# Performance work log

Hardware: AMD Instinct MI355X
Metric: run time of the kernel (lower is better)

Reference implementation:

```python
import jax, jax.numpy as jnp
import numpy as np

D_MODEL = 1024

def setup_inputs() -> dict:
    key = jax.random.key(0)
    k1, k2, kU, kb, kw, kfb = jax.random.split(key, 6)
    B, S, d = 8, 2048, D_MODEL
    x1 = jax.random.normal(k1, (B, S, d), dtype=jnp.float32)
    x2 = jax.random.normal(k2, (B, S, d), dtype=jnp.float32)
    U = jax.random.normal(kU, (d, d), dtype=jnp.float32) * (1.0 / np.sqrt(d))
    bias = jax.random.normal(kb, (d,), dtype=jnp.float32) * 0.02
    fc_w = jax.random.normal(kw, (d // 2, d), dtype=jnp.float32) * (1.0 / np.sqrt(d))
    fc_b = jnp.zeros((d // 2,), dtype=jnp.float32)
    return {"x1": x1, "x2": x2, "U": U, "bias": bias, "fc_w": fc_w, "fc_b": fc_b}

def reference(x1, x2, U, bias, fc_w, fc_b):
    # attn scores: (x2 @ U) @ x1^T  -> [B, S2, S1]
    attn = jnp.einsum("bsd,de,bte->bst", x2, U, x1)
    # additive bias per key position: x1 @ bias -> [B, 1, S1]
    attn = attn + jnp.einsum("btd,d->bt", x1, bias)[:, None, :]
    attn = jax.nn.softmax(attn, axis=-1)
    # dropout is identity in eval mode
    out = jnp.einsum("bst,btd->bsd", attn, x1)
    out = jnp.einsum("bsd,ed->bse", out, fc_w) + fc_b
    return jax.nn.relu(out)
```

## Files before the change

### kernel.cpp

```cpp
#include <hip/hip_runtime.h>
#include <hip/hip_fp16.h>
#include <cstddef>
#include <cstdint>

typedef _Float16 f16;
typedef _Float16 f16x8 __attribute__((ext_vector_type(8)));
typedef _Float16 f16x4 __attribute__((ext_vector_type(4)));
typedef float    f32x4 __attribute__((ext_vector_type(4)));

#define BK 64

__device__ __forceinline__ void gload16(const void* g, void* lds) {
  __builtin_amdgcn_global_load_lds(
      (const __attribute__((address_space(1))) unsigned int*)g,
      (__attribute__((address_space(3))) unsigned int*)lds, 16, 0, 0);
}

template<int R>
__device__ __forceinline__ void stage_f16(f16 (*buf)[BK], const f16* __restrict__ src,
                                          int ld, int w, int lane) {
#pragma unroll
  for (int i = 0; i < R / 32; i++) {
    const int grp  = w * (R / 32) + i;
    const int r    = grp * 8 + (lane >> 3);
    const int slot = (lane & 7) ^ (r & 7);
    gload16(src + (size_t)r * ld + slot * 8, &buf[grp * 8][0]);
  }
}

template<int R>
struct RegStage {
  static constexpr int NV = (R == 128) ? 8 : 4;
  float4 v[NV];
  __device__ __forceinline__ void load(const float* __restrict__ src, int ld, int tid) {
    const int r = (R == 128) ? (tid >> 1) : (tid >> 2);
    const int h = (R == 128) ? (tid & 1) * 32 : (tid & 3) * 16;
    const float* p = src + (size_t)r * ld + h;
#pragma unroll
    for (int j = 0; j < NV; j++) v[j] = ((const float4*)p)[j];
  }
  __device__ __forceinline__ void write(f16 (*buf)[BK], int tid) {
    const int r = (R == 128) ? (tid >> 1) : (tid >> 2);
    const int h = (R == 128) ? (tid & 1) * 32 : (tid & 3) * 16;
#pragma unroll
    for (int g = 0; g < NV / 2; g++) {
      const float4 a = v[g * 2], b = v[g * 2 + 1];
      f16x8 o;
      o[0] = (f16)a.x; o[1] = (f16)a.y; o[2] = (f16)a.z; o[3] = (f16)a.w;
      o[4] = (f16)b.x; o[5] = (f16)b.y; o[6] = (f16)b.z; o[7] = (f16)b.w;
      const int slot = (h / 8 + g) ^ (r & 7);
      *(f16x8*)&buf[r][slot * 8] = o;
    }
  }
};

template<int BMt, int BNt, typename TA, typename TB, bool BIAS, bool RELU, typename TC>
__global__ __launch_bounds__(256, 2)
void gemm_tn(const TA* __restrict__ A, int lda,
             const TB* __restrict__ B, int ldb,
             TC* __restrict__ C, int ldc,
             const float* __restrict__ bias, int K)
{
  constexpr int MF = BMt / 32;
  constexpr int NF = BNt / 32;
  __shared__ f16 As[2][BMt][BK];
  __shared__ f16 Bs[2][BNt][BK];
  const int tid  = threadIdx.x;
  const int lane = tid & 63;
  const int w    = tid >> 6;
  const int wr   = w >> 1, wc = w & 1;

  const int gx = gridDim.x, nxy = gx * gridDim.y;
  int lin = blockIdx.y * gx + blockIdx.x;
  lin = (lin & 7) * (nxy >> 3) + (lin >> 3);
  const int m0 = (lin % gx) * BMt;
  const int n0 = (lin / gx) * BNt;

  f32x4 acc[MF][NF] = {};
  RegStage<BMt> ra;
  RegStage<BNt> rb;

  auto stage_issue = [&](int buf, int k0) {
    if constexpr (sizeof(TA) == 2)
      stage_f16<BMt>(As[buf], (const f16*)A + (size_t)m0 * lda + k0, lda, w, lane);
    else
      ra.load((const float*)A + (size_t)m0 * lda + k0, lda, tid);
    if constexpr (sizeof(TB) == 2)
      stage_f16<BNt>(Bs[buf], (const f16*)B + (size_t)n0 * ldb + k0, ldb, w, lane);
    else
      rb.load((const float*)B + (size_t)n0 * ldb + k0, ldb, tid);
  };
  auto stage_write = [&](int buf) {
    if constexpr (sizeof(TA) == 4) ra.write(As[buf], tid);
    if constexpr (sizeof(TB) == 4) rb.write(Bs[buf], tid);
  };
  auto compute = [&](int buf) {
    const int fr = lane & 15, q = lane >> 4;
#pragma unroll
    for (int kk = 0; kk < 2; kk++) {
      f16x8 af[MF], bf[NF];
#pragma unroll
      for (int i = 0; i < MF; i++) {
        const int r = wr * (BMt / 2) + i * 16 + fr;
        const int slot = (kk * 4 + q) ^ (r & 7);
        af[i] = *(const f16x8*)&As[buf][r][slot * 8];
      }
#pragma unroll
      for (int j = 0; j < NF; j++) {
        const int r = wc * (BNt / 2) + j * 16 + fr;
        const int slot = (kk * 4 + q) ^ (r & 7);
        bf[j] = *(const f16x8*)&Bs[buf][r][slot * 8];
      }
#pragma unroll
      for (int i = 0; i < MF; i++)
#pragma unroll
        for (int j = 0; j < NF; j++)
          acc[i][j] = __builtin_amdgcn_mfma_f32_16x16x32_f16(af[i], bf[j], acc[i][j], 0, 0, 0);
    }
  };

  stage_issue(0, 0);
  stage_write(0);
  __syncthreads();

  const int KT = K / BK;
  for (int kt = 0; kt < KT; kt++) {
    const int cur = kt & 1, nxt = cur ^ 1;
    if (kt + 1 < KT) stage_issue(nxt, (kt + 1) * BK);
    compute(cur);
    if (kt + 1 < KT) stage_write(nxt);
    __syncthreads();
  }

  const int fr = lane & 15;
  const int rg = (lane >> 4) << 2;
#pragma unroll
  for (int i = 0; i < MF; i++) {
#pragma unroll
    for (int j = 0; j < NF; j++) {
      const int col = n0 + wc * (BNt / 2) + j * 16 + fr;
      float bv = 0.f;
      if constexpr (BIAS) bv = bias[col];
#pragma unroll
      for (int r = 0; r < 4; r++) {
        const int row = m0 + wr * (BMt / 2) + i * 16 + rg + r;
        float v = acc[i][j][r] + bv;
        if constexpr (RELU) v = fmaxf(v, 0.f);
        C[(size_t)row * ldc + col] = (TC)v;
      }
    }
  }
}

__global__ __launch_bounds__(256)
void copy_f32_f16(const float* __restrict__ in, f16* __restrict__ o)
{
  const size_t i = ((size_t)blockIdx.x * 256 + threadIdx.x) * 8;
  const float4 a = ((const float4*)(in + i))[0];
  const float4 b = ((const float4*)(in + i))[1];
  f16x8 v;
  v[0] = (f16)a.x; v[1] = (f16)a.y; v[2] = (f16)a.z; v[3] = (f16)a.w;
  v[4] = (f16)b.x; v[5] = (f16)b.y; v[6] = (f16)b.z; v[7] = (f16)b.w;
  *(f16x8*)(o + i) = v;
}

__global__ __launch_bounds__(256)
void bias_dot(const float* __restrict__ x1, const float* __restrict__ bias,
              float* __restrict__ bT)
{
  const int row  = blockIdx.x * 4 + (threadIdx.x >> 6);
  const int lane = threadIdx.x & 63;
  const float4* r = (const float4*)(x1 + (size_t)row * 1024);
  const float4* bb = (const float4*)bias;
  float acc = 0.f;
#pragma unroll
  for (int j = 0; j < 4; j++) {
    const float4 a = r[lane + j * 64];
    const float4 b = bb[lane + j * 64];
    acc += a.x * b.x + a.y * b.y + a.z * b.z + a.w * b.w;
  }
#pragma unroll
  for (int off = 32; off > 0; off >>= 1) acc += __shfl_xor(acc, off);
  if (lane == 0) bT[row] = acc;
}

__global__ __launch_bounds__(256)
void softmax_rows(float* __restrict__ S)
{
  float* row = S + (size_t)blockIdx.x * 2048;
  const int t = threadIdx.x;
  const float4 v0 = ((const float4*)row)[t];
  const float4 v1 = ((const float4*)row)[t + 256];

  float m = fmaxf(fmaxf(fmaxf(v0.x, v0.y), fmaxf(v0.z, v0.w)),
                  fmaxf(fmaxf(v1.x, v1.y), fmaxf(v1.z, v1.w)));
#pragma unroll
  for (int off = 32; off > 0; off >>= 1) m = fmaxf(m, __shfl_xor(m, off));
  __shared__ float red[8];
  if ((t & 63) == 0) red[t >> 6] = m;
  __syncthreads();
  m = fmaxf(fmaxf(red[0], red[1]), fmaxf(red[2], red[3]));

  float e0 = __expf(v0.x - m), e1 = __expf(v0.y - m), e2 = __expf(v0.z - m), e3 = __expf(v0.w - m);
  float e4 = __expf(v1.x - m), e5 = __expf(v1.y - m), e6 = __expf(v1.z - m), e7 = __expf(v1.w - m);
  float s = ((e0 + e1) + (e2 + e3)) + ((e4 + e5) + (e6 + e7));
#pragma unroll
  for (int off = 32; off > 0; off >>= 1) s += __shfl_xor(s, off);
  if ((t & 63) == 0) red[4 + (t >> 6)] = s;
  __syncthreads();
  const float inv = 1.f / (red[4] + red[5] + red[6] + red[7]);

  f16x4 o0, o1;
  o0[0] = (f16)(e0 * inv); o0[1] = (f16)(e1 * inv); o0[2] = (f16)(e2 * inv); o0[3] = (f16)(e3 * inv);
  o1[0] = (f16)(e4 * inv); o1[1] = (f16)(e5 * inv); o1[2] = (f16)(e6 * inv); o1[3] = (f16)(e7 * inv);
  f16x4* orow = (f16x4*)row;
  orow[t]       = o0;
  orow[t + 256] = o1;
}

extern "C" void kernel_launch(void* const* d_in, const int* in_sizes, int n_in,
                              void* d_out, int out_size, void* d_ws, size_t ws_size,
                              hipStream_t stream)
{
  const float* x1   = (const float*)d_in[0];
  const float* x2   = (const float*)d_in[1];
  const float* U    = (const float*)d_in[2];
  const float* bias = (const float*)d_in[3];
  const float* fcw  = (const float*)d_in[4];
  const float* fcb  = (const float*)d_in[5];
  float* out = (float*)d_out;

  const int S = 2048, D = 1024, E = 512, B = 8;
  const size_t MB = 1ull << 20;
  const size_t KB64 = 64 * 1024;

  const bool FULL = ws_size >= (4 * MB + KB64 + 16 * MB);

  char* w = (char*)d_ws;
  f16*   W2  = (f16*)(w);
  f16*   W1Tf = (f16*)(w + 4 * MB);
  float* bT  = FULL ? (float*)(w + 4 * MB) : (float*)(w + 6 * MB);
  float* Sb  = FULL ? (float*)(w + 4 * MB + KB64) : (float*)(w + 6 * MB + KB64);
  f16*   Uh  = (f16*)(w + 14 * MB + KB64);
  f16*   Fh  = (f16*)(w + 16 * MB + KB64);

  const int SC = FULL ? 2048 : 1024;

  f16* X2h = (f16*)d_out;

  copy_f32_f16<<<dim3(B * S * D / 2048), 256, 0, stream>>>(x2, X2h);
  bias_dot<<<dim3(B * S / 4), 256, 0, stream>>>(x1, bias, bT);
  if (!FULL) {
    copy_f32_f16<<<dim3(D * D / 2048), 256, 0, stream>>>(U, Uh);
    copy_f32_f16<<<dim3(E * D / 2048), 256, 0, stream>>>(fcw, Fh);
  }

  for (int b = 0; b < B; b++) {
    const float* x1b = x1 + (size_t)b * S * D;
    const f16*   X2b = X2h + (size_t)b * S * D;

    if (FULL) {
      gemm_tn<64, 128, float, float, false, false, f16><<<dim3(S / 64, D / 128), 256, 0, stream>>>(
          x1b, D, U, D, W2, D, nullptr, D);

      gemm_tn<64, 128, f16, f16, true, false, float><<<dim3(S / 64, S / 128), 256, 0, stream>>>(
          X2b, D, W2, D, Sb, S, bT + (size_t)b * S, D);

      softmax_rows<<<dim3(S), 256, 0, stream>>>(Sb);

      gemm_tn<64, 128, float, float, false, false, f16><<<dim3(E / 64, S / 128), 256, 0, stream>>>(
          fcw, D, x1b, D, (f16*)Sb + 2048, 2 * S, nullptr, D);

      gemm_tn<64, 64, f16, f16, true, true, float><<<dim3(S / 64, E / 64), 256, 0, stream>>>(
          (const f16*)Sb, 2 * S, (const f16*)Sb + 2048, 2 * S,
          out + (size_t)b * S * E, E, fcb, S);
    } else {
      gemm_tn<64, 128, float, f16, false, false, f16><<<dim3(S / 64, D / 128), 256, 0, stream>>>(
          x1b, D, Uh, D, W2, D, nullptr, D);

      gemm_tn<64, 64, f16, float, false, false, f16><<<dim3(E / 64, S / 64), 256, 0, stream>>>(
          Fh, D, x1b, D, W1Tf, S, nullptr, D);

      for (int s0 = 0; s0 < S; s0 += SC) {
        gemm_tn<64, 128, f16, f16, true, false, float><<<dim3(SC / 64, S / 128), 256, 0, stream>>>(
            X2b + (size_t)s0 * D, D, W2, D, Sb, S, bT + (size_t)b * S, D);
        softmax_rows<<<dim3(SC), 256, 0, stream>>>(Sb);
        gemm_tn<64, 64, f16, f16, true, true, float><<<dim3(SC / 64, E / 64), 256, 0, stream>>>(
            (const f16*)Sb, 2 * S, W1Tf, S, out + ((size_t)b * S + s0) * E, E, fcb, S);
      }
    }
  }
}
```

Measured before the change: 825.7 us.

## Pre-convert U to fp16, enlarge score GEMM tile, retile fc GEMM

In the full-workspace path, U is now converted to fp16 once per batch by a fused copy kernel, so the x1·U GEMM reads fp16 B operands instead of fp32. The score GEMM moves from 64x128 to 128x128 tiles for more operand reuse per block, and the fc_w·x1 GEMM uses 64x64 tiles for more blocks. The non-full path merges its two conversion kernels into one launch. Risks: the larger tile halves the grid and may lower occupancy, and U is reconverted on every batch iteration.

```diff
diff --git a/kernel.cpp b/kernel.cpp
--- a/kernel.cpp
+++ b/kernel.cpp
@@ -165,6 +165,23 @@
 }
 
 __global__ __launch_bounds__(256)
+void copy_uf(const float* __restrict__ U, const float* __restrict__ fcw,
+             f16* __restrict__ Uh, f16* __restrict__ Fh)
+{
+  const bool isU = blockIdx.x < 512;
+  const size_t base = (size_t)(isU ? blockIdx.x : blockIdx.x - 512) * 2048;
+  const float* in = (isU ? U : fcw) + base;
+  f16* o = (isU ? Uh : Fh) + base;
+  const size_t i = (size_t)threadIdx.x * 8;
+  const float4 a = ((const float4*)(in + i))[0];
+  const float4 b = ((const float4*)(in + i))[1];
+  f16x8 v;
+  v[0] = (f16)a.x; v[1] = (f16)a.y; v[2] = (f16)a.z; v[3] = (f16)a.w;
+  v[4] = (f16)b.x; v[5] = (f16)b.y; v[6] = (f16)b.z; v[7] = (f16)b.w;
+  *(f16x8*)(o + i) = v;
+}
+
+__global__ __launch_bounds__(256)
 void bias_dot(const float* __restrict__ x1, const float* __restrict__ bias,
               float* __restrict__ bT)
 {
@@ -237,55 +254,52 @@
   const bool FULL = ws_size >= (4 * MB + KB64 + 16 * MB);
 
   char* w = (char*)d_ws;
-  f16*   W2  = (f16*)(w);
+  f16*   W2   = (f16*)(w);
   f16*   W1Tf = (f16*)(w + 4 * MB);
-  float* bT  = FULL ? (float*)(w + 4 * MB) : (float*)(w + 6 * MB);
-  float* Sb  = FULL ? (float*)(w + 4 * MB + KB64) : (float*)(w + 6 * MB + KB64);
-  f16*   Uh  = (f16*)(w + 14 * MB + KB64);
-  f16*   Fh  = (f16*)(w + 16 * MB + KB64);
-
-  const int SC = FULL ? 2048 : 1024;
+  float* bT   = FULL ? (float*)(w + 4 * MB) : (float*)(w + 6 * MB);
+  float* Sb   = FULL ? (float*)(w + 4 * MB + KB64) : (float*)(w + 6 * MB + KB64);
+  f16*   Uh   = FULL ? (f16*)((char*)Sb + 13 * MB) : (f16*)(w + 14 * MB + KB64);
+  f16*   Fh   = (f16*)(w + 16 * MB + KB64);
+  f16*   W1T  = FULL ? (f16*)Sb + 2048 : W1Tf;
+  const int ldw1t = FULL ? 2 * S : S;
 
   f16* X2h = (f16*)d_out;
 
   copy_f32_f16<<<dim3(B * S * D / 2048), 256, 0, stream>>>(x2, X2h);
   bias_dot<<<dim3(B * S / 4), 256, 0, stream>>>(x1, bias, bT);
-  if (!FULL) {
-    copy_f32_f16<<<dim3(D * D / 2048), 256, 0, stream>>>(U, Uh);
-    copy_f32_f16<<<dim3(E * D / 2048), 256, 0, stream>>>(fcw, Fh);
-  }
+  if (!FULL)
+    copy_uf<<<dim3(768), 256, 0, stream>>>(U, fcw, Uh, Fh);
 
   for (int b = 0; b < B; b++) {
     const float* x1b = x1 + (size_t)b * S * D;
     const f16*   X2b = X2h + (size_t)b * S * D;
 
     if (FULL) {
-      gemm_tn<64, 128, float, float, false, false, f16><<<dim3(S / 64, D / 128), 256, 0, stream>>>(
-          x1b, D, U, D, W2, D, nullptr, D);
-
-      gemm_tn<64, 128, f16, f16, true, false, float><<<dim3(S / 64, S / 128), 256, 0, stream>>>(
+      copy_uf<<<dim3(512), 256, 0, stream>>>(U, fcw, Uh, nullptr);
+
+      gemm_tn<64, 128, float, f16, false, false, f16><<<dim3(S / 64, D / 128), 256, 0, stream>>>(
+          x1b, D, Uh, D, W2, D, nullptr, D);
+
+      gemm_tn<128, 128, f16, f16, true, false, float><<<dim3(S / 128, S / 128), 256, 0, stream>>>(
           X2b, D, W2, D, Sb, S, bT + (size_t)b * S, D);
 
       softmax_rows<<<dim3(S), 256, 0, stream>>>(Sb);
 
-      gemm_tn<64, 128, float, float, false, false, f16><<<dim3(E / 64, S / 128), 256, 0, stream>>>(
-          fcw, D, x1b, D, (f16*)Sb + 2048, 2 * S, nullptr, D);
+      gemm_tn<64, 64, float, float, false, false, f16><<<dim3(E / 64, S / 64), 256, 0, stream>>>(
+          fcw, D, x1b, D, W1T, ldw1t, nullptr, D);
 
       gemm_tn<64, 64, f16, f16, true, true, float><<<dim3(S / 64, E / 64), 256, 0, stream>>>(
-          (const f16*)Sb, 2 * S, (const f16*)Sb + 2048, 2 * S,
-          out + (size_t)b * S * E, E, fcb, S);
+          (const f16*)Sb, 2 * S, W1T, ldw1t, out + (size_t)b * S * E, E, fcb, S);
     } else {
       gemm_tn<64, 128, float, f16, false, false, f16><<<dim3(S / 64, D / 128), 256, 0, stream>>>(
           x1b, D, Uh, D, W2, D, nullptr, D);
-
       gemm_tn<64, 64, f16, float, false, false, f16><<<dim3(E / 64, S / 64), 256, 0, stream>>>(
           Fh, D, x1b, D, W1Tf, S, nullptr, D);
-
-      for (int s0 = 0; s0 < S; s0 += SC) {
-        gemm_tn<64, 128, f16, f16, true, false, float><<<dim3(SC / 64, S / 128), 256, 0, stream>>>(
+      for (int s0 = 0; s0 < S; s0 += 1024) {
+        gemm_tn<64, 128, f16, f16, true, false, float><<<dim3(1024 / 64, S / 128), 256, 0, stream>>>(
             X2b + (size_t)s0 * D, D, W2, D, Sb, S, bT + (size_t)b * S, D);
-        softmax_rows<<<dim3(SC), 256, 0, stream>>>(Sb);
-        gemm_tn<64, 64, f16, f16, true, true, float><<<dim3(SC / 64, E / 64), 256, 0, stream>>>(
+        softmax_rows<<<dim3(1024), 256, 0, stream>>>(Sb);
+        gemm_tn<64, 64, f16, f16, true, true, float><<<dim3(1024 / 64, E / 64), 256, 0, stream>>>(
             (const f16*)Sb, 2 * S, W1Tf, S, out + ((size_t)b * S + s0) * E, E, fcb, S);
       }
     }
```

Measured after the change: 721.5 us. 1.14x faster.
